# Kernel tuning notes

Hardware: AMD Instinct MI355X
Metric: run time of the kernel (lower is better)

The kernel has to match this reference:

```python
import jax, jax.numpy as jnp
import numpy as np

N, E, D, H, C, B, G = 50000, 800000, 128, 256, 40, 3, 2
EPS = 1e-5


def setup_inputs() -> dict:
    key = jax.random.key(0)
    ks = jax.random.split(key, 32)
    rn = lambda k, s: jax.random.normal(k, s, dtype=jnp.float32)
    inp = {
        'x': rn(ks[0], (N, D)),
        'edge_index': jax.random.randint(ks[1], (2, E), 0, N, dtype=jnp.int64),
        'Wp': rn(ks[2], (D, H)), 'bp': rn(ks[3], (H,)),
        'W1l': rn(ks[4], (B, H, H)), 'b1l': rn(ks[5], (B, H)), 'W1r': rn(ks[6], (B, H, H)),
        'W2l': rn(ks[7], (B, H, H)), 'b2l': rn(ks[8], (B, H)), 'W2r': rn(ks[9], (B, H, H)),
        'bn1_g': rn(ks[10], (B, H)), 'bn1_b': rn(ks[11], (B, H)), 'bn1_m': rn(ks[12], (B, H)),
        'bn1_v': jax.random.uniform(ks[13], (B, H), dtype=jnp.float32),
        'bn2_g': rn(ks[14], (B, H)), 'bn2_b': rn(ks[15], (B, H)), 'bn2_m': rn(ks[16], (B, H)),
        'bn2_v': jax.random.uniform(ks[17], (B, H), dtype=jnp.float32),
        'gate_W': rn(ks[18], (G, H, H)), 'gate_b': rn(ks[19], (G, H)),
        'Wc1': rn(ks[20], (H, H // 2)), 'bc1': rn(ks[21], (H // 2,)),
        'Wc2': rn(ks[22], (H // 2, C)), 'bc2': rn(ks[23], (C,)),
    }
    return inp


def _sage(x, src, dst, Wl, bl, Wr):
    # PyG SAGEConv (mean aggr): lin_l(mean_{j in N(i)} x_j) + lin_r(x_i)
    agg = jax.ops.segment_sum(x[src], dst, num_segments=N)  # [N,H]
    cnt = jax.ops.segment_sum(jnp.ones((src.shape[0],), x.dtype), dst, num_segments=N)
    mean = agg / jnp.maximum(cnt, 1.0)[:, None]
    return mean @ Wl + bl + x @ Wr


def _bn(x, g, b, m, v):
    return (x - m) * (g * jax.lax.rsqrt(v + EPS)) + b


def reference(x, edge_index, Wp, bp, W1l, b1l, W1r, W2l, b2l, W2r,
              bn1_g, bn1_b, bn1_m, bn1_v, bn2_g, bn2_b, bn2_m, bn2_v,
              gate_W, gate_b, Wc1, bc1, Wc2, bc2):
    src, dst = edge_index[0], edge_index[1]
    prev = x @ Wp + bp  # input projection [N,H]
    for i in range(B):
        res = prev
        h = jax.nn.relu(_bn(_sage(prev, src, dst, W1l[i], b1l[i], W1r[i]),
                            bn1_g[i], bn1_b[i], bn1_m[i], bn1_v[i]))
        h = jax.nn.relu(_bn(_sage(h, src, dst, W2l[i], b2l[i], W2r[i]),
                            bn2_g[i], bn2_b[i], bn2_m[i], bn2_v[i]))
        cur = h + res
        if i > 0:
            gate = jax.nn.sigmoid(prev @ gate_W[i - 1] + gate_b[i - 1])
            cur = gate * prev + (1.0 - gate) * cur
        prev = cur
    return jax.nn.relu(prev @ Wc1 + bc1) @ Wc2 + bc2  # [N,C]
```

## Files before the change

### kernel.cpp

```cpp
#include <hip/hip_runtime.h>
#include <hip/hip_bf16.h>
#include <cstdint>

#define NNODES 50000
#define MPAD   50048
#define NEDGES 800000
#define DIN 128
#define HID 256
#define NCLS 40
#define NBLK 3
#define EPSV 1e-5f

typedef __bf16 bf16x8 __attribute__((ext_vector_type(8)));
typedef float  f32x4  __attribute__((ext_vector_type(4)));
typedef unsigned short us4v __attribute__((ext_vector_type(4)));
typedef unsigned short us8v __attribute__((ext_vector_type(8)));

__device__ __forceinline__ unsigned short bf_rtn(float x) {
  unsigned u = __float_as_uint(x);
  return (unsigned short)((u + 0x7fffu + ((u >> 16) & 1u)) >> 16);
}
__device__ __forceinline__ float bf_f(unsigned short h) {
  return __uint_as_float((unsigned)h << 16);
}
__device__ __forceinline__ void split4(float4 a, us4v& h, us4v& m, us4v& l) {
  float v[4] = {a.x, a.y, a.z, a.w};
#pragma unroll
  for (int i = 0; i < 4; i++) {
    unsigned short hh = bf_rtn(v[i]);
    float r1 = v[i] - bf_f(hh);
    unsigned short mm = bf_rtn(r1);
    float r2 = r1 - bf_f(mm);
    h[i] = hh; m[i] = mm; l[i] = bf_rtn(r2);
  }
}

__device__ __forceinline__ void glds16(const void* gsrc, void* ldst) {
  __builtin_amdgcn_global_load_lds((const __attribute__((address_space(1))) void*)gsrc,
                                   (__attribute__((address_space(3))) void*)ldst,
                                   16, 0, 0);
}

__global__ void hist_kernel(const int* __restrict__ dst, int* __restrict__ cnt, int E) {
  int e = blockIdx.x * blockDim.x + threadIdx.x;
  if (e < E) atomicAdd(&cnt[dst[e]], 1);
}

__global__ void scan_kernel(const int* __restrict__ cnt, int* __restrict__ row_ptr,
                            float* __restrict__ inv_cnt, int N) {
  __shared__ int sums[1024];
  int t = threadIdx.x;
  int chunk = (N + 1023) >> 10;
  int beg = t * chunk;
  int end = beg + chunk; if (end > N) end = N;
  int s = 0;
  for (int i = beg; i < end; ++i) s += cnt[i];
  sums[t] = s;
  __syncthreads();
  for (int off = 1; off < 1024; off <<= 1) {
    int v = 0;
    if (t >= off) v = sums[t - off];
    __syncthreads();
    sums[t] += v;
    __syncthreads();
  }
  int run = (t == 0) ? 0 : sums[t - 1];
  for (int i = beg; i < end; ++i) {
    row_ptr[i] = run;
    int c = cnt[i];
    inv_cnt[i] = 1.0f / (float)(c > 0 ? c : 1);
    run += c;
  }
  if (t == 1023) row_ptr[N] = run;
}

__global__ void fill_kernel(const int* __restrict__ src, const int* __restrict__ dst,
                            const int* __restrict__ row_ptr, int* __restrict__ fillc,
                            int* __restrict__ col, int E) {
  int e = blockIdx.x * blockDim.x + threadIdx.x;
  if (e < E) {
    int d = dst[e];
    int pos = atomicAdd(&fillc[d], 1);
    col[row_ptr[d] + pos] = src[e];
  }
}

__global__ __launch_bounds__(256)
void agg_kernel(const float* __restrict__ x, float* __restrict__ out,
                const int* __restrict__ row_ptr, const int* __restrict__ col,
                const float* __restrict__ inv_cnt) {
  int n = blockIdx.x;
  int h = threadIdx.x;
  int beg = row_ptr[n], end = row_ptr[n + 1];
  float s = 0.0f;
  for (int j = beg; j < end; ++j) {
    int c = col[j];
    s += x[(long)c * HID + h];
  }
  out[(long)n * HID + h] = s * inv_cnt[n];
}

__global__ void fold_kernel(const float* __restrict__ b1l, const float* __restrict__ g1,
                            const float* __restrict__ bb1, const float* __restrict__ m1,
                            const float* __restrict__ v1,
                            const float* __restrict__ b2l, const float* __restrict__ g2,
                            const float* __restrict__ bb2, const float* __restrict__ m2,
                            const float* __restrict__ v2,
                            float* __restrict__ S1, float* __restrict__ T1,
                            float* __restrict__ S2, float* __restrict__ T2) {
  int idx = blockIdx.x * 256 + threadIdx.x;
  float s1 = g1[idx] * rsqrtf(v1[idx] + EPSV);
  S1[idx] = s1;
  T1[idx] = (b1l[idx] - m1[idx]) * s1 + bb1[idx];
  float s2 = g2[idx] * rsqrtf(v2[idx] + EPSV);
  S2[idx] = s2;
  T2[idx] = (b2l[idx] - m2[idx]) * s2 + bb2[idx];
}

#define PREP_TOTAL 368640
struct PrepDescs {
  const float* src[16];
  unsigned dst_off[16];
  int N[16];
  int cum[16];
};
__global__ __launch_bounds__(256)
void prep_kernel(PrepDescs pd, char* out) {
  int i = blockIdx.x * 256 + threadIdx.x;
  if (i >= PREP_TOTAL) return;
  int j = 0;
  while (i >= pd.cum[j]) j++;
  int li = i - (j ? pd.cum[j - 1] : 0);
  int c = li % 12;
  int t = li / 12;
  int N = pd.N[j];
  int n = t % N;
  int kt = t / N;
  const float* src = pd.src[j];
  char* base = out + pd.dst_off[j] + (size_t)kt * N * 192;
  int p, k8;
  size_t addr;
  if (c < 8) {
    int d = c ^ (n & 7);
    p = d >> 2; k8 = d & 3;
    addr = (size_t)n * 128 + (size_t)c * 16;
  } else {
    p = 2; k8 = c - 8;
    addr = (size_t)N * 128 + ((size_t)k8 * N + n) * 16;
  }
  us8v v;
#pragma unroll
  for (int xj = 0; xj < 8; xj++) {
    float w = src[(size_t)(kt * 32 + k8 * 8 + xj) * N + n];
    unsigned short h = bf_rtn(w);
    if (p == 0) { v[xj] = h; continue; }
    float r1 = w - bf_f(h);
    unsigned short m = bf_rtn(r1);
    v[xj] = (p == 1) ? m : bf_rtn(r1 - bf_f(m));
  }
  *reinterpret_cast<us8v*>(base + addr) = v;
}

template<bool GATED>
__global__ __launch_bounds__(256)
void gemm_mfma(const float* __restrict__ A1, const char* __restrict__ B1, int K1,
               const float* __restrict__ A2, const char* __restrict__ B2, int K2,
               const char* __restrict__ BG, const float* __restrict__ Gb,
               const float* __restrict__ Sc, const float* __restrict__ Tc,
               const float* __restrict__ resid, float* __restrict__ C,
               int Bn, int Mguard, int do_relu) {
  __shared__ __align__(16) unsigned short A_lds[2][64][104];
  __shared__ __align__(16) char B_lds[2][24576];
  const int tid  = threadIdx.x;
  const int wv   = tid >> 6;
  const int lane = tid & 63;
  const int l15  = lane & 15;
  const int quad = lane >> 4;
  const int NC   = Bn >> 7;
  const int n0   = (blockIdx.x % NC) * 128;
  const int m0   = (blockIdx.x / NC) * 64;
  const int wm   = wv >> 1;
  const int wn   = wv & 1;
  const int sr   = tid >> 3;
  const int skc  = (tid & 7) * 4;

  f32x4 acc1[2][4];
#pragma unroll
  for (int i = 0; i < 2; i++)
#pragma unroll
    for (int j = 0; j < 4; j++) acc1[i][j] = (f32x4){0.f, 0.f, 0.f, 0.f};
  f32x4 acc2[GATED ? 2 : 1][GATED ? 4 : 1];
  if constexpr (GATED) {
#pragma unroll
    for (int i = 0; i < 2; i++)
#pragma unroll
      for (int j = 0; j < 4; j++) acc2[i][j] = (f32x4){0.f, 0.f, 0.f, 0.f};
  }

  int buf = 0;

  auto issueB = [&](const char* Bp, int kt, int b) {
    const char* tb = Bp + (size_t)kt * ((size_t)Bn * 192);
#pragma unroll
    for (int j = 0; j < 6; ++j) {
      int o = wv * 6144 + j * 1024;
      const char* src;
      if (o < 16384) {
        src = tb + (size_t)n0 * 128 + o;
      } else {
        int ol = o - 16384;
        int k8 = ol >> 11;
        int within = ol & 2047;
        src = tb + (size_t)Bn * 128 + (size_t)k8 * Bn * 16 + (size_t)n0 * 16 + within;
      }
      glds16(src + (size_t)lane * 16, &B_lds[b][o]);
    }
  };
  auto storeA = [&](float4 (&a)[2], int b) {
#pragma unroll
    for (int i = 0; i < 2; i++) {
      us4v h4, m4, l4;
      split4(a[i], h4, m4, l4);
      unsigned short* rp = &A_lds[b][sr + i * 32][0];
      *reinterpret_cast<us4v*>(rp + skc)      = h4;
      *reinterpret_cast<us4v*>(rp + 32 + skc) = m4;
      *reinterpret_cast<us4v*>(rp + 64 + skc) = l4;
    }
  };

  auto phase = [&](const float* __restrict__ A, const char* __restrict__ Bp,
                   int K, f32x4 (&acc)[2][4]) {
    const int KT = K / 32;
    bool g[2];
    const float* ap[2];
#pragma unroll
    for (int i = 0; i < 2; i++) {
      int row = m0 + sr + i * 32;
      g[i] = row < Mguard;
      ap[i] = A + (size_t)row * K + skc;
    }
    issueB(Bp, 0, buf);
    {
      float4 a[2];
#pragma unroll
      for (int i = 0; i < 2; i++)
        a[i] = g[i] ? *reinterpret_cast<const float4*>(ap[i]) : make_float4(0.f, 0.f, 0.f, 0.f);
      storeA(a, buf);
    }
    for (int kt = 0; kt < KT; ++kt) {
      __syncthreads();
      bf16x8 ah[2], am[2], al[2];
#pragma unroll
      for (int mt = 0; mt < 2; mt++) {
        const unsigned short* rp = &A_lds[buf][wm * 32 + mt * 16 + l15][0];
        ah[mt] = *reinterpret_cast<const bf16x8*>(rp + quad * 8);
        am[mt] = *reinterpret_cast<const bf16x8*>(rp + 32 + quad * 8);
        al[mt] = *reinterpret_cast<const bf16x8*>(rp + 64 + quad * 8);
      }
      bf16x8 bh[4], bm_[4], bl[4];
#pragma unroll
      for (int nt = 0; nt < 4; nt++) {
        int ln = wn * 64 + nt * 16 + l15;
        int sw = ln & 7;
        const char* rb = &B_lds[buf][(size_t)ln * 128];
        bh[nt]  = *reinterpret_cast<const bf16x8*>(rb + ((quad ^ sw) * 16));
        bm_[nt] = *reinterpret_cast<const bf16x8*>(rb + (((4 + quad) ^ sw) * 16));
        bl[nt]  = *reinterpret_cast<const bf16x8*>(
            &B_lds[buf][16384 + ((size_t)quad * 128 + ln) * 16]);
      }
      const bool pf = (kt + 1 < KT);
      float4 a[2];
      if (pf) {
        issueB(Bp, kt + 1, buf ^ 1);
#pragma unroll
        for (int i = 0; i < 2; i++)
          a[i] = g[i] ? *reinterpret_cast<const float4*>(ap[i] + (kt + 1) * 32)
                      : make_float4(0.f, 0.f, 0.f, 0.f);
      }
#pragma unroll
      for (int nt = 0; nt < 4; nt++) {
#pragma unroll
        for (int mt = 0; mt < 2; mt++) {
          acc[mt][nt] = __builtin_amdgcn_mfma_f32_16x16x32_bf16(ah[mt], bh[nt],  acc[mt][nt], 0, 0, 0);
          acc[mt][nt] = __builtin_amdgcn_mfma_f32_16x16x32_bf16(ah[mt], bm_[nt], acc[mt][nt], 0, 0, 0);
          acc[mt][nt] = __builtin_amdgcn_mfma_f32_16x16x32_bf16(am[mt], bh[nt],  acc[mt][nt], 0, 0, 0);
          acc[mt][nt] = __builtin_amdgcn_mfma_f32_16x16x32_bf16(am[mt], bm_[nt], acc[mt][nt], 0, 0, 0);
          acc[mt][nt] = __builtin_amdgcn_mfma_f32_16x16x32_bf16(ah[mt], bl[nt],  acc[mt][nt], 0, 0, 0);
          acc[mt][nt] = __builtin_amdgcn_mfma_f32_16x16x32_bf16(al[mt], bh[nt],  acc[mt][nt], 0, 0, 0);
        }
      }
      if (pf) storeA(a, buf ^ 1);
      buf ^= 1;
    }
  };

  phase(A1, B1, K1, acc1);
  if (A2) phase(A2, B2, K2, acc1);
  if constexpr (GATED) phase(resid, BG, HID, acc2);

#pragma unroll
  for (int nt = 0; nt < 4; nt++) {
    int colc = n0 + wn * 64 + nt * 16 + l15;
    float sc = Sc ? Sc[colc] : 1.0f;
    float tc = Tc[colc];
    float gb = 0.0f;
    if constexpr (GATED) gb = Gb[colc];
#pragma unroll
    for (int mt = 0; mt < 2; mt++) {
#pragma unroll
      for (int r = 0; r < 4; r++) {
        int row = m0 + wm * 32 + mt * 16 + quad * 4 + r;
        size_t base = (size_t)row * Bn + colc;
        float v = acc1[mt][nt][r] * sc + tc;
        if (do_relu) v = fmaxf(v, 0.0f);
        if constexpr (GATED) {
          float p = resid[base];
          float g = 1.0f / (1.0f + __expf(-(acc2[mt][nt][r] + gb)));
          v = g * p + (1.0f - g) * (v + p);
        } else if (resid) {
          v += resid[base];
        }
        C[base] = v;
      }
    }
  }
}

__global__ __launch_bounds__(256)
void classifier2(const float* __restrict__ Tin, const float* __restrict__ W,
                 const float* __restrict__ bias, float* __restrict__ out, int M) {
  __shared__ float Ws[DIN * NCLS];
  __shared__ float bs[NCLS];
  __shared__ float Ts[64][DIN + 4];
  int tid = threadIdx.x;
  for (int i = tid; i < DIN * NCLS; i += 256) Ws[i] = W[i];
  if (tid < NCLS) bs[tid] = bias[tid];
  int row0 = blockIdx.x * 64;
  for (int idx = tid; idx < 64 * (DIN / 4); idx += 256) {
    int r = idx / (DIN / 4);
    int c4 = idx % (DIN / 4);
    float4 v = make_float4(0.f, 0.f, 0.f, 0.f);
    if (row0 + r < M) v = *reinterpret_cast<const float4*>(Tin + (long)(row0 + r) * DIN + c4 * 4);
    *reinterpret_cast<float4*>(&Ts[r][c4 * 4]) = v;
  }
  __syncthreads();
  int r = tid >> 2;
  int c0 = (tid & 3) * 10;
  float s[10];
#pragma unroll
  for (int c = 0; c < 10; c++) s[c] = bs[c0 + c];
  for (int k = 0; k < DIN; k++) {
    float a = Ts[r][k];
#pragma unroll
    for (int c = 0; c < 10; c++) s[c] = fmaf(a, Ws[k * NCLS + c0 + c], s[c]);
  }
  if (row0 + r < M) {
#pragma unroll
    for (int c = 0; c < 10; c++) out[(long)(row0 + r) * NCLS + c0 + c] = s[c];
  }
}

extern "C" void kernel_launch(void* const* d_in, const int* in_sizes, int n_in,
                              void* d_out, int out_size, void* d_ws, size_t ws_size,
                              hipStream_t stream) {
  const float* x      = (const float*)d_in[0];
  const int*   ei     = (const int*)d_in[1];
  const float* Wp     = (const float*)d_in[2];
  const float* bp     = (const float*)d_in[3];
  const float* W1l    = (const float*)d_in[4];
  const float* b1l    = (const float*)d_in[5];
  const float* W1r    = (const float*)d_in[6];
  const float* W2l    = (const float*)d_in[7];
  const float* b2l    = (const float*)d_in[8];
  const float* W2r    = (const float*)d_in[9];
  const float* bn1_g  = (const float*)d_in[10];
  const float* bn1_b  = (const float*)d_in[11];
  const float* bn1_m  = (const float*)d_in[12];
  const float* bn1_v  = (const float*)d_in[13];
  const float* bn2_g  = (const float*)d_in[14];
  const float* bn2_b  = (const float*)d_in[15];
  const float* bn2_m  = (const float*)d_in[16];
  const float* bn2_v  = (const float*)d_in[17];
  const float* gate_W = (const float*)d_in[18];
  const float* gate_b = (const float*)d_in[19];
  const float* Wc1    = (const float*)d_in[20];
  const float* bc1    = (const float*)d_in[21];
  const float* Wc2    = (const float*)d_in[22];
  const float* bc2    = (const float*)d_in[23];
  const int* srcp = ei;
  const int* dstp = ei + NEDGES;

  char* wsb = (char*)d_ws;
  size_t off = 0;
  auto alloc = [&](size_t bytes) -> void* {
    void* p = wsb + off;
    off += (bytes + 255) & ~(size_t)255;
    return p;
  };
  float* X0 = (float*)alloc((size_t)MPAD * HID * 4);
  float* X1 = (float*)alloc((size_t)MPAD * HID * 4);
  float* X2 = (float*)alloc((size_t)MPAD * HID * 4);
  float* X3 = (float*)alloc((size_t)MPAD * HID * 4);
  char* prep = (char*)alloc(5898240);
  int* cnt     = (int*)alloc((size_t)NNODES * 4 * 2);
  int* fillc   = cnt + NNODES;
  int* row_ptr = (int*)alloc((size_t)(NNODES + 1) * 4);
  float* inv   = (float*)alloc((size_t)NNODES * 4);
  int* col     = (int*)alloc((size_t)NEDGES * 4);
  float* S1 = (float*)alloc(NBLK * HID * 4);
  float* T1 = (float*)alloc(NBLK * HID * 4);
  float* S2 = (float*)alloc(NBLK * HID * 4);
  float* T2 = (float*)alloc(NBLK * HID * 4);

  auto poff = [](int idx) -> unsigned {
    if (idx == 0) return 0;
    return 196608u + (unsigned)(idx - 1) * 393216u;
  };
  const char* prepWp  = prep + poff(0);
  auto prepW1l = [&](int i) { return prep + poff(1 + i); };
  auto prepW1r = [&](int i) { return prep + poff(4 + i); };
  auto prepW2l = [&](int i) { return prep + poff(7 + i); };
  auto prepW2r = [&](int i) { return prep + poff(10 + i); };
  auto prepGate = [&](int g) { return prep + poff(13 + g); };
  const char* prepWc1 = prep + poff(15);

  PrepDescs pd;
  {
    int c = 0, k = 0;
    auto add = [&](const float* s, int N, int chunks, unsigned doff) {
      pd.src[k] = s; pd.N[k] = N; c += chunks; pd.cum[k] = c; pd.dst_off[k] = doff; k++;
    };
    add(Wp, 256, 12288, poff(0));
    for (int i = 0; i < 3; i++) add(W1l + (size_t)i * 65536, 256, 24576, poff(1 + i));
    for (int i = 0; i < 3; i++) add(W1r + (size_t)i * 65536, 256, 24576, poff(4 + i));
    for (int i = 0; i < 3; i++) add(W2l + (size_t)i * 65536, 256, 24576, poff(7 + i));
    for (int i = 0; i < 3; i++) add(W2r + (size_t)i * 65536, 256, 24576, poff(10 + i));
    for (int g = 0; g < 2; g++) add(gate_W + (size_t)g * 65536, 256, 24576, poff(13 + g));
    add(Wc1, 128, 12288, poff(15));
  }

  hipMemsetAsync(cnt, 0, (size_t)NNODES * 4 * 2, stream);
  int eb = (NEDGES + 255) / 256;
  hist_kernel<<<eb, 256, 0, stream>>>(dstp, cnt, NEDGES);
  scan_kernel<<<1, 1024, 0, stream>>>(cnt, row_ptr, inv, NNODES);
  fill_kernel<<<eb, 256, 0, stream>>>(srcp, dstp, row_ptr, fillc, col, NEDGES);
  fold_kernel<<<3, 256, 0, stream>>>(b1l, bn1_g, bn1_b, bn1_m, bn1_v,
                                     b2l, bn2_g, bn2_b, bn2_m, bn2_v, S1, T1, S2, T2);
  prep_kernel<<<PREP_TOTAL / 256, 256, 0, stream>>>(pd, prep);

  const int gmw = MPAD / 64;
  const int g256 = gmw * 2;
  gemm_mfma<false><<<g256, 256, 0, stream>>>(
      x, prepWp, DIN, nullptr, nullptr, 0, nullptr, nullptr,
      nullptr, bp, nullptr, X0, 256, NNODES, 0);

  float* bufs[4] = {X0, X1, X2, X3};
  int ip = 0;
  for (int i = 0; i < NBLK; ++i) {
    int im = (ip + 1) & 3;
    int ih = (ip + 2) & 3;
    int id = (ip + 3) & 3;
    float* P  = bufs[ip];
    float* Mb = bufs[im];
    float* Hb = bufs[ih];
    float* Db = bufs[id];
    agg_kernel<<<NNODES, 256, 0, stream>>>(P, Mb, row_ptr, col, inv);
    gemm_mfma<false><<<g256, 256, 0, stream>>>(
        Mb, prepW1l(i), HID, P, prepW1r(i), HID, nullptr, nullptr,
        S1 + i * HID, T1 + i * HID, nullptr, Hb, 256, MPAD, 1);
    agg_kernel<<<NNODES, 256, 0, stream>>>(Hb, Mb, row_ptr, col, inv);
    if (i == 0) {
      gemm_mfma<false><<<g256, 256, 0, stream>>>(
          Mb, prepW2l(0), HID, Hb, prepW2r(0), HID, nullptr, nullptr,
          S2, T2, P, Db, 256, MPAD, 1);
    } else {
      gemm_mfma<true><<<g256, 256, 0, stream>>>(
          Mb, prepW2l(i), HID, Hb, prepW2r(i), HID,
          prepGate(i - 1), gate_b + (size_t)(i - 1) * HID,
          S2 + i * HID, T2 + i * HID, P, Db, 256, MPAD, 1);
    }
    ip = id;
  }
  float* P  = bufs[ip];
  float* Tb = bufs[(ip + 1) & 3];
  gemm_mfma<false><<<gmw, 256, 0, stream>>>(
      P, prepWc1, HID, nullptr, nullptr, 0, nullptr, nullptr,
      nullptr, bc1, nullptr, Tb, 128, MPAD, 1);
  classifier2<<<gmw, 256, 0, stream>>>(Tb, Wc2, bc2, (float*)d_out, NNODES);
}
```

Baseline: 2.107 ms.

## Store aggregated features pre-split into bf16 planes in GEMM tile layout

The aggregation kernel now writes its mean output directly as hi/mid/lo bf16 planes, laid out to match the GEMM's LDS A-tile. The GEMM then loads that operand with direct global-to-LDS copies instead of loading fp32 and splitting it in registers. This removes the per-tile split arithmetic and LDS stores from the GEMM's first phase. In exchange, the aggregation kernel does scattered 2-byte stores and the split work moves into it. A workspace-size check selects between the new path and the old fp32 path.

New measurement: 2.183 ms. +3.6%, slower.

```diff
diff --git a/kernel.cpp b/kernel.cpp
--- a/kernel.cpp
+++ b/kernel.cpp
@@ -4,6 +4,7 @@
 
 #define NNODES 50000
 #define MPAD   50048
+#define NROWT  782
 #define NEDGES 800000
 #define DIN 128
 #define HID 256
@@ -33,6 +34,18 @@
     float r2 = r1 - bf_f(mm);
     h[i] = hh; m[i] = mm; l[i] = bf_rtn(r2);
   }
+}
+
+__device__ __forceinline__ void plane_store(char* base, int KT, int r, int c, float v) {
+  size_t o = ((size_t)((r >> 6) * KT + (c >> 5))) * 12288
+           + (size_t)(((c >> 3) & 3) * 1024 + (r & 63) * 16 + (c & 7) * 2);
+  unsigned short h = bf_rtn(v);
+  float r1 = v - bf_f(h);
+  unsigned short m = bf_rtn(r1);
+  unsigned short l = bf_rtn(r1 - bf_f(m));
+  *(unsigned short*)(base + o)        = h;
+  *(unsigned short*)(base + o + 4096) = m;
+  *(unsigned short*)(base + o + 8192) = l;
 }
 
 __device__ __forceinline__ void glds16(const void* gsrc, void* ldst) {
@@ -86,7 +99,8 @@
 }
 
 __global__ __launch_bounds__(256)
-void agg_kernel(const float* __restrict__ x, float* __restrict__ out,
+void agg_kernel(const float* __restrict__ x, float* __restrict__ outf,
+                char* __restrict__ outp,
                 const int* __restrict__ row_ptr, const int* __restrict__ col,
                 const float* __restrict__ inv_cnt) {
   int n = blockIdx.x;
@@ -97,7 +111,9 @@
     int c = col[j];
     s += x[(long)c * HID + h];
   }
-  out[(long)n * HID + h] = s * inv_cnt[n];
+  float v = s * inv_cnt[n];
+  if (outp) plane_store(outp, 8, n, h, v);
+  else      outf[(long)n * HID + h] = v;
 }
 
 __global__ void fold_kernel(const float* __restrict__ b1l, const float* __restrict__ g1,
@@ -163,13 +179,15 @@
 
 template<bool GATED>
 __global__ __launch_bounds__(256)
-void gemm_mfma(const float* __restrict__ A1, const char* __restrict__ B1, int K1,
-               const float* __restrict__ A2, const char* __restrict__ B2, int K2,
-               const char* __restrict__ BG, const float* __restrict__ Gb,
+void gemm_mfma(const char* __restrict__ A1p, const float* __restrict__ A1f,
+               const char* __restrict__ B1, int K1,
+               const float* __restrict__ A2f, const char* __restrict__ B2, int K2,
+               const float* __restrict__ AGf, const char* __restrict__ BG,
+               const float* __restrict__ Gb,
                const float* __restrict__ Sc, const float* __restrict__ Tc,
                const float* __restrict__ resid, float* __restrict__ C,
                int Bn, int Mguard, int do_relu) {
-  __shared__ __align__(16) unsigned short A_lds[2][64][104];
+  __shared__ __align__(16) char A_lds[2][12288];
   __shared__ __align__(16) char B_lds[2][24576];
   const int tid  = threadIdx.x;
   const int wv   = tid >> 6;
@@ -179,10 +197,12 @@
   const int NC   = Bn >> 7;
   const int n0   = (blockIdx.x % NC) * 128;
   const int m0   = (blockIdx.x / NC) * 64;
+  const int rt   = m0 >> 6;
   const int wm   = wv >> 1;
   const int wn   = wv & 1;
   const int sr   = tid >> 3;
-  const int skc  = (tid & 7) * 4;
+  const int c0   = (tid & 7) * 4;
+  const int aoff = ((c0 >> 3) & 3) * 1024 + (c0 & 7) * 2;
 
   f32x4 acc1[2][4];
 #pragma unroll
@@ -199,6 +219,13 @@
 
   int buf = 0;
 
+  auto issueApl = [&](const char* Ap, int KT, int kt, int b) {
+    const char* src = Ap + ((size_t)(rt * KT + kt)) * 12288 + wv * 3072 + (size_t)lane * 16;
+    char* dst = &A_lds[b][wv * 3072];
+#pragma unroll
+    for (int j = 0; j < 3; ++j)
+      glds16(src + j * 1024, dst + j * 1024);
+  };
   auto issueB = [&](const char* Bp, int kt, int b) {
     const char* tb = Bp + (size_t)kt * ((size_t)Bn * 192);
 #pragma unroll
@@ -221,26 +248,31 @@
     for (int i = 0; i < 2; i++) {
       us4v h4, m4, l4;
       split4(a[i], h4, m4, l4);
-      unsigned short* rp = &A_lds[b][sr + i * 32][0];
-      *reinterpret_cast<us4v*>(rp + skc)      = h4;
-      *reinterpret_cast<us4v*>(rp + 32 + skc) = m4;
-      *reinterpret_cast<us4v*>(rp + 64 + skc) = l4;
+      char* p0 = &A_lds[b][(size_t)(sr + i * 32) * 16 + aoff];
+      *reinterpret_cast<us4v*>(p0)        = h4;
+      *reinterpret_cast<us4v*>(p0 + 4096) = m4;
+      *reinterpret_cast<us4v*>(p0 + 8192) = l4;
     }
   };
 
-  auto phase = [&](const float* __restrict__ A, const char* __restrict__ Bp,
+  auto phase = [&](const char* Apl, const float* Af, const char* Bp,
                    int K, f32x4 (&acc)[2][4]) {
     const int KT = K / 32;
+    const bool pl = (Apl != nullptr);
     bool g[2];
     const float* ap[2];
-#pragma unroll
-    for (int i = 0; i < 2; i++) {
-      int row = m0 + sr + i * 32;
-      g[i] = row < Mguard;
-      ap[i] = A + (size_t)row * K + skc;
+    if (!pl) {
+#pragma unroll
+      for (int i = 0; i < 2; i++) {
+        int row = m0 + sr + i * 32;
+        g[i] = row < Mguard;
+        ap[i] = Af + (size_t)row * K + c0;
+      }
     }
     issueB(Bp, 0, buf);
-    {
+    if (pl) {
+      issueApl(Apl, KT, 0, buf);
+    } else {
       float4 a[2];
 #pragma unroll
       for (int i = 0; i < 2; i++)
@@ -252,10 +284,10 @@
       bf16x8 ah[2], am[2], al[2];
 #pragma unroll
       for (int mt = 0; mt < 2; mt++) {
-        const unsigned short* rp = &A_lds[buf][wm * 32 + mt * 16 + l15][0];
-        ah[mt] = *reinterpret_cast<const bf16x8*>(rp + quad * 8);
-        am[mt] = *reinterpret_cast<const bf16x8*>(rp + 32 + quad * 8);
-        al[mt] = *reinterpret_cast<const bf16x8*>(rp + 64 + quad * 8);
+        const char* ra = &A_lds[buf][quad * 1024 + (size_t)(wm * 32 + mt * 16 + l15) * 16];
+        ah[mt] = *reinterpret_cast<const bf16x8*>(ra);
+        am[mt] = *reinterpret_cast<const bf16x8*>(ra + 4096);
+        al[mt] = *reinterpret_cast<const bf16x8*>(ra + 8192);
       }
       bf16x8 bh[4], bm_[4], bl[4];
 #pragma unroll
@@ -272,10 +304,14 @@
       float4 a[2];
       if (pf) {
         issueB(Bp, kt + 1, buf ^ 1);
-#pragma unroll
-        for (int i = 0; i < 2; i++)
-          a[i] = g[i] ? *reinterpret_cast<const float4*>(ap[i] + (kt + 1) * 32)
-                      : make_float4(0.f, 0.f, 0.f, 0.f);
+        if (pl) {
+          issueApl(Apl, KT, kt + 1, buf ^ 1);
+        } else {
+#pragma unroll
+          for (int i = 0; i < 2; i++)
+            a[i] = g[i] ? *reinterpret_cast<const float4*>(ap[i] + (kt + 1) * 32)
+                        : make_float4(0.f, 0.f, 0.f, 0.f);
+        }
       }
 #pragma unroll
       for (int nt = 0; nt < 4; nt++) {
@@ -289,14 +325,14 @@
           acc[mt][nt] = __builtin_amdgcn_mfma_f32_16x16x32_bf16(al[mt], bh[nt],  acc[mt][nt], 0, 0, 0);
         }
       }
-      if (pf) storeA(a, buf ^ 1);
+      if (pf && !pl) storeA(a, buf ^ 1);
       buf ^= 1;
     }
   };
 
-  phase(A1, B1, K1, acc1);
-  if (A2) phase(A2, B2, K2, acc1);
-  if constexpr (GATED) phase(resid, BG, HID, acc2);
+  phase(A1p, A1f, B1, K1, acc1);
+  if (A2f) phase(nullptr, A2f, B2, K2, acc1);
+  if constexpr (GATED) phase(nullptr, AGf, BG, HID, acc2);
 
 #pragma unroll
   for (int nt = 0; nt < 4; nt++) {
@@ -397,11 +433,24 @@
     off += (bytes + 255) & ~(size_t)255;
     return p;
   };
-  float* X0 = (float*)alloc((size_t)MPAD * HID * 4);
-  float* X1 = (float*)alloc((size_t)MPAD * HID * 4);
-  float* X2 = (float*)alloc((size_t)MPAD * HID * 4);
-  float* X3 = (float*)alloc((size_t)MPAD * HID * 4);
-  char* prep = (char*)alloc(5898240);
+  const size_t XFSZ = (size_t)MPAD * HID * 4;
+  const size_t MPSZ = (size_t)NROWT * 8 * 12288;
+  const bool big = (ws_size >= 241000000ull);
+
+  float* R[4] = {nullptr, nullptr, nullptr, nullptr};
+  char* Mp = nullptr;
+  if (big) {
+    R[0] = (float*)alloc(XFSZ);
+    R[1] = (float*)alloc(XFSZ);
+    R[2] = (float*)alloc(XFSZ);
+    Mp   = (char*)alloc(MPSZ);
+  } else {
+    R[0] = (float*)alloc(XFSZ);
+    R[1] = (float*)alloc(XFSZ);
+    R[2] = (float*)alloc(XFSZ);
+    R[3] = (float*)alloc(XFSZ);
+  }
+  char* prep   = (char*)alloc(5898240);
   int* cnt     = (int*)alloc((size_t)NNODES * 4 * 2);
   int* fillc   = cnt + NNODES;
   int* row_ptr = (int*)alloc((size_t)(NNODES + 1) * 4);
@@ -448,43 +497,64 @@
                                      b2l, bn2_g, bn2_b, bn2_m, bn2_v, S1, T1, S2, T2);
   prep_kernel<<<PREP_TOTAL / 256, 256, 0, stream>>>(pd, prep);
 
-  const int gmw = MPAD / 64;
-  const int g256 = gmw * 2;
+  const int gmw  = NROWT;
+  const int g256 = NROWT * 2;
+  float* Tb = nullptr;
+
   gemm_mfma<false><<<g256, 256, 0, stream>>>(
-      x, prepWp, DIN, nullptr, nullptr, 0, nullptr, nullptr,
-      nullptr, bp, nullptr, X0, 256, NNODES, 0);
-
-  float* bufs[4] = {X0, X1, X2, X3};
-  int ip = 0;
-  for (int i = 0; i < NBLK; ++i) {
-    int im = (ip + 1) & 3;
-    int ih = (ip + 2) & 3;
-    int id = (ip + 3) & 3;
-    float* P  = bufs[ip];
-    float* Mb = bufs[im];
-    float* Hb = bufs[ih];
-    float* Db = bufs[id];
-    agg_kernel<<<NNODES, 256, 0, stream>>>(P, Mb, row_ptr, col, inv);
-    gemm_mfma<false><<<g256, 256, 0, stream>>>(
-        Mb, prepW1l(i), HID, P, prepW1r(i), HID, nullptr, nullptr,
-        S1 + i * HID, T1 + i * HID, nullptr, Hb, 256, MPAD, 1);
-    agg_kernel<<<NNODES, 256, 0, stream>>>(Hb, Mb, row_ptr, col, inv);
-    if (i == 0) {
+      nullptr, x, prepWp, DIN, nullptr, nullptr, 0, nullptr, nullptr, nullptr,
+      nullptr, bp, nullptr, R[0], 256, NNODES, 0);
+
+  if (big) {
+    int p = 0, h = 1, d = 2;
+    for (int i = 0; i < NBLK; ++i) {
+      agg_kernel<<<NNODES, 256, 0, stream>>>(R[p], nullptr, Mp, row_ptr, col, inv);
       gemm_mfma<false><<<g256, 256, 0, stream>>>(
-          Mb, prepW2l(0), HID, Hb, prepW2r(0), HID, nullptr, nullptr,
-          S2, T2, P, Db, 256, MPAD, 1);
-    } else {
-      gemm_mfma<true><<<g256, 256, 0, stream>>>(
-          Mb, prepW2l(i), HID, Hb, prepW2r(i), HID,
-          prepGate(i - 1), gate_b + (size_t)(i - 1) * HID,
-          S2 + i * HID, T2 + i * HID, P, Db, 256, MPAD, 1);
-    }
-    ip = id;
-  }
-  float* P  = bufs[ip];
-  float* Tb = bufs[(ip + 1) & 3];
-  gemm_mfma<false><<<gmw, 256, 0, stream>>>(
-      P, prepWc1, HID, nullptr, nullptr, 0, nullptr, nullptr,
-      nullptr, bc1, nullptr, Tb, 128, MPAD, 1);
+          Mp, nullptr, prepW1l(i), HID, R[p], prepW1r(i), HID, nullptr, nullptr, nullptr,
+          S1 + i * HID, T1 + i * HID, nullptr, R[h], 256, MPAD, 1);
+      agg_kernel<<<NNODES, 256, 0, stream>>>(R[h], nullptr, Mp, row_ptr, col, inv);
+      if (i == 0) {
+        gemm_mfma<false><<<g256, 256, 0, stream>>>(
+            Mp, nullptr, prepW2l(0), HID, R[h], prepW2r(0), HID, nullptr, nullptr, nullptr,
+            S2, T2, R[p], R[d], 256, MPAD, 1);
+      } else {
+        gemm_mfma<true><<<g256, 256, 0, stream>>>(
+            Mp, nullptr, prepW2l(i), HID, R[h], prepW2r(i), HID,
+            R[p], prepGate(i - 1), gate_b + (size_t)(i - 1) * HID,
+            S2 + i * HID, T2 + i * HID, R[p], R[d], 256, MPAD, 1);
+      }
+      int np = d, nh = p, nd = h;
+      p = np; h = nh; d = nd;
+    }
+    Tb = R[h];
+    gemm_mfma<false><<<gmw, 256, 0, stream>>>(
+        nullptr, R[p], prepWc1, HID, nullptr, nullptr, 0, nullptr, nullptr, nullptr,
+        nullptr, bc1, nullptr, Tb, 128, MPAD, 1);
+  } else {
+    int ip = 0;
+    for (int i = 0; i < NBLK; ++i) {
+      int im = (ip + 1) & 3, ih = (ip + 2) & 3, id = (ip + 3) & 3;
+      agg_kernel<<<NNODES, 256, 0, stream>>>(R[ip], R[im], nullptr, row_ptr, col, inv);
+      gemm_mfma<false><<<g256, 256, 0, stream>>>(
+          nullptr, R[im], prepW1l(i), HID, R[ip], prepW1r(i), HID, nullptr, nullptr, nullptr,
+          S1 + i * HID, T1 + i * HID, nullptr, R[ih], 256, MPAD, 1);
+      agg_kernel<<<NNODES, 256, 0, stream>>>(R[ih], R[im], nullptr, row_ptr, col, inv);
+      if (i == 0) {
+        gemm_mfma<false><<<g256, 256, 0, stream>>>(
+            nullptr, R[im], prepW2l(0), HID, R[ih], prepW2r(0), HID, nullptr, nullptr, nullptr,
+            S2, T2, R[ip], R[id], 256, MPAD, 1);
+      } else {
+        gemm_mfma<true><<<g256, 256, 0, stream>>>(
+            nullptr, R[im], prepW2l(i), HID, R[ih], prepW2r(i), HID,
+            R[ip], prepGate(i - 1), gate_b + (size_t)(i - 1) * HID,
+            S2 + i * HID, T2 + i * HID, R[ip], R[id], 256, MPAD, 1);
+      }
+      ip = id;
+    }
+    Tb = R[(ip + 1) & 3];
+    gemm_mfma<false><<<gmw, 256, 0, stream>>>(
+        nullptr, R[ip], prepWc1, HID, nullptr, nullptr, 0, nullptr, nullptr, nullptr,
+        nullptr, bc1, nullptr, Tb, 128, MPAD, 1);
+  }
   classifier2<<<gmw, 256, 0, stream>>>(Tb, Wc2, bc2, (float*)d_out, NNODES);
 }
```
